# Performance work log

Measured on AMD Instinct MI355X. Metric: run time of the kernel, lower is better.

## Reference

```python
import jax, jax.numpy as jnp
import numpy as np

NUM_EMBEDDINGS = 1024
EMBED_DIM = 256
EMA_DECAY = 0.99
EPS = 1e-05


def setup_inputs() -> dict:
    key = jax.random.key(0)
    k1, k2, k3 = jax.random.split(key, 3)
    B, D, H, W = 32, EMBED_DIM, 32, 32
    z = jax.random.normal(k1, (B, D, H, W), dtype=jnp.float32)
    # torch init: uniform(-1/K, 1/K)
    scale = 1.0 / NUM_EMBEDDINGS
    embedding = jax.random.uniform(k2, (NUM_EMBEDDINGS, EMBED_DIM), dtype=jnp.float32,
                                   minval=-scale, maxval=scale)
    ema_cluster_size = jnp.zeros((NUM_EMBEDDINGS,), dtype=jnp.float32)
    # buffer initialized to a copy of the embedding weights
    ema_embed_sum = embedding.copy()
    return {"z": z, "embedding": embedding,
            "ema_cluster_size": ema_cluster_size, "ema_embed_sum": ema_embed_sum}


def reference(z, embedding, ema_cluster_size, ema_embed_sum):
    B, D, H, W = z.shape
    K = embedding.shape[0]
    # (B, D, H, W) -> (N, D) with N = B*H*W
    z_flat = jnp.transpose(z, (0, 2, 3, 1)).reshape(-1, D)
    # squared L2 distances: ||z||^2 - 2 z E^T + ||e||^2  -> (N, K)
    distances = (jnp.sum(z_flat * z_flat, axis=1, keepdims=True)
                 - 2.0 * z_flat @ embedding.T
                 + jnp.sum(embedding * embedding, axis=1)[None, :])
    indices = jnp.argmin(distances, axis=1)  # (N,) int32
    z_q = embedding[indices].reshape(B, H, W, D).transpose(0, 3, 1, 2)  # (B, D, H, W)

    # training-mode EMA updates (pure functional: return new buffers / codebook)
    ones = jnp.ones((z_flat.shape[0],), dtype=z_flat.dtype)
    counts = jax.ops.segment_sum(ones, indices, num_segments=K)          # (K,)
    embed_sum = jax.ops.segment_sum(z_flat, indices, num_segments=K)     # (K, D)
    new_cs = EMA_DECAY * ema_cluster_size + (1.0 - EMA_DECAY) * counts
    new_es = EMA_DECAY * ema_embed_sum + (1.0 - EMA_DECAY) * embed_sum
    n = jnp.sum(new_cs)
    cluster_size = (new_cs + EPS) / (n + K * EPS) * n
    new_embedding = new_es / cluster_size[:, None]

    # commitment loss and straight-through estimator
    commitment_loss = jnp.mean((z - jax.lax.stop_gradient(z_q)) ** 2)
    z_q_st = z + jax.lax.stop_gradient(z_q - z)
    indices_grid = indices.reshape(B, H, W)
    return (z_q_st, commitment_loss, indices_grid, new_embedding, new_cs, new_es)
```

## Files before the change

kernel.cpp:

```cpp
#include <hip/hip_runtime.h>

#define D_  256
#define K_  1024
#define HW_ 1024
#define N_  32768

#define WS_COUNTS  262144
#define WS_EMBSUM  266240
#define WS_LOSS    1314816
#define WS_NSUM    1314820
#define WS_ENMAX   1314824
#define WS_ZERO0   262144
#define WS_ZEROLEN 1052684
#define WS_NEWCS   1314828
#define WS_ENORM   1318924
#define WS_E16     1454096
#define WS_TOTAL   1978384

#define O_ZQ   0
#define O_LOSS 8388608
#define O_IDX  8388609
#define O_EMB  8421377
#define O_NCS  8683521
#define O_NES  8684545

typedef unsigned short u16;
typedef _Float16 f16x8 __attribute__((ext_vector_type(8)));
typedef float f32x4 __attribute__((ext_vector_type(4)));

__device__ __forceinline__ unsigned f16x2pack(float a, float b) {
  union { _Float16 h; unsigned short u; } ca, cb;
  ca.h = (_Float16)a; cb.h = (_Float16)b;
  return (unsigned)ca.u | ((unsigned)cb.u << 16);
}

__device__ __forceinline__ float pw256_sq(const float* __restrict__ p, int stride) {
  float tot0 = 0.f, tot1 = 0.f;
#pragma unroll
  for (int h = 0; h < 2; ++h) {
    const float* q = p + h * 128 * stride;
    float r[8];
#pragma unroll
    for (int j = 0; j < 8; ++j) { float x = q[j * stride]; r[j] = __fmul_rn(x, x); }
    for (int i = 8; i < 128; i += 8)
#pragma unroll
      for (int j = 0; j < 8; ++j) {
        float x = q[(i + j) * stride];
        r[j] = __fadd_rn(r[j], __fmul_rn(x, x));
      }
    float s = __fadd_rn(__fadd_rn(__fadd_rn(r[0], r[1]), __fadd_rn(r[2], r[3])),
                        __fadd_rn(__fadd_rn(r[4], r[5]), __fadd_rn(r[6], r[7])));
    if (h == 0) tot0 = s; else tot1 = s;
  }
  return __fadd_rn(tot0, tot1);
}

__global__ void vq_eprep(const float* __restrict__ E, float* __restrict__ enorm,
                         u16* __restrict__ E16, unsigned* __restrict__ enmax) {
  int k = blockIdx.x * 256 + threadIdx.x;
  float v = pw256_sq(E + k * D_, 1);
  enorm[k] = v;
  atomicMax(enmax, __float_as_uint(v));
  unsigned* E16w = (unsigned*)E16;
  for (int wd = k; wd < (K_ * D_ / 2); wd += 1024) {
    float2 x = *(const float2*)(E + 2 * wd);
    E16w[wd] = f16x2pack(512.0f * x.x, 512.0f * x.y);
  }
}

template <int CTRL>
__device__ __forceinline__ float dppmin(float v) {
  int p = __builtin_amdgcn_update_dpp(0, __float_as_int(v), CTRL, 0xF, 0xF, true);
  return fminf(v, __int_as_float(p));
}

__device__ __forceinline__ void exact_update(
    const float* zrow, const float* __restrict__ E, int t, int c,
    const float* zn_s, const float* en_s, unsigned long long* best_s) {
  const float* ep = E + c * D_;
  float a = 0.f;
  for (int d0 = 0; d0 < 256; d0 += 8) {
    f32x4 z0 = *(const f32x4*)(zrow + d0);
    f32x4 z1 = *(const f32x4*)(zrow + d0 + 4);
    float4 e0 = *(const float4*)(ep + d0);
    float4 e1 = *(const float4*)(ep + d0 + 4);
    a = __fmaf_rn(z0[0], e0.x, a); a = __fmaf_rn(z0[1], e0.y, a);
    a = __fmaf_rn(z0[2], e0.z, a); a = __fmaf_rn(z0[3], e0.w, a);
    a = __fmaf_rn(z1[0], e1.x, a); a = __fmaf_rn(z1[1], e1.y, a);
    a = __fmaf_rn(z1[2], e1.z, a); a = __fmaf_rn(z1[3], e1.w, a);
  }
  float s = __fadd_rn(__fsub_rn(zn_s[t], __fmul_rn(2.0f, a)), en_s[c]);
  unsigned long long key = ((unsigned long long)__float_as_uint(s) << 32) | (unsigned)c;
  atomicMin(&best_s[t], key);
}

#define TCAP 96
#define ZP  260

__global__ __launch_bounds__(256, 4) void vq_main(
    const float* __restrict__ z, const float* __restrict__ E,
    const u16* __restrict__ E16, const float* __restrict__ enorm,
    const unsigned* __restrict__ enmax,
    float* __restrict__ embsum, float* __restrict__ loss_sum,
    float* __restrict__ counts, float* __restrict__ out_zq,
    float* __restrict__ out_idx) {
  __shared__ __align__(16) float zs[32 * ZP];
  __shared__ float en_s[K_];
  __shared__ float zn_s[32];
  __shared__ float mg_s[32];
  __shared__ unsigned rmin_s[32];
  __shared__ unsigned long long best_s[32];
  __shared__ unsigned tcount[4];
  __shared__ unsigned tlist[4][TCAP];
  __shared__ float wred[4];

  const int tid = threadIdx.x;
  const int tile = blockIdx.x;
  const int bimg = tile >> 5;
  const int hw0 = (tile & 31) << 5;
  const float* zb = z + bimg * (D_ * HW_) + hw0;
  const int n0 = bimg * HW_ + hw0;

#pragma unroll
  for (int r = 0; r < 8; ++r) {
    int ii = r * 256 + tid;
    int d = ii >> 3, t4 = (ii & 7) * 4;
    float4 v = *(const float4*)(zb + d * HW_ + t4);
    zs[(t4 + 0) * ZP + d] = v.x; zs[(t4 + 1) * ZP + d] = v.y;
    zs[(t4 + 2) * ZP + d] = v.z; zs[(t4 + 3) * ZP + d] = v.w;
  }
  for (int i = tid; i < K_; i += 256) en_s[i] = enorm[i];
  if (tid < 4) tcount[tid] = 0;
  __syncthreads();
  if (tid < 32) {
    float zn = pw256_sq(&zs[tid * ZP], 1);
    zn_s[tid] = zn;
    float em = __uint_as_float(*enmax);
    mg_s[tid] = 0.00390625f * sqrtf(zn * em) + 5e-4f;
    rmin_s[tid] = 0xFFFFFFFFu;
    best_s[tid] = ~0ull;
  }
  __syncthreads();

  const int lane = tid & 63;
  const int w = tid >> 6;
  const int l15 = lane & 15, g = lane >> 4;
  const int cw = w * 256;
  const u16* Eb = E16 + (unsigned)(cw + l15) * D_ + g * 8;

  f16x8 efA[2], efB[2];
#pragma unroll
  for (int n = 0; n < 2; ++n)
    efA[n] = *(const f16x8*)(Eb + n * 16 * D_);

  f32x4 acc[2][2];

#define MSTEP(S, EFU, EFF, SN)                                                   \
  {                                                                              \
    const int kk_ = (S) & 7;                                                     \
    {                                                                            \
      const int cn_ = (SN) >> 3, kn_ = (SN) & 7;                                 \
      _Pragma("unroll")                                                          \
      for (int n = 0; n < 2; ++n)                                                \
        EFF[n] = *(const f16x8*)(Eb + (cn_ * 32 + n * 16) * D_ + kn_ * 32);      \
    }                                                                            \
    f16x8 zf_[2];                                                                \
    _Pragma("unroll")                                                            \
    for (int m = 0; m < 2; ++m) {                                                \
      const float* zr = zs + (m * 16 + l15) * ZP + kk_ * 32 + g * 8;             \
      f32x4 lo = *(const f32x4*)zr;                                              \
      f32x4 hi = *(const f32x4*)(zr + 4);                                        \
      f16x8 zc;                                                                  \
      _Pragma("unroll")                                                          \
      for (int j = 0; j < 4; ++j) {                                              \
        zc[j] = (_Float16)lo[j]; zc[4 + j] = (_Float16)hi[j];                    \
      }                                                                          \
      zf_[m] = zc;                                                               \
    }                                                                            \
    _Pragma("unroll")                                                            \
    for (int m = 0; m < 2; ++m)                                                  \
      _Pragma("unroll")                                                          \
      for (int n = 0; n < 2; ++n)                                                \
        acc[m][n] = __builtin_amdgcn_mfma_f32_16x16x32_f16(zf_[m], EFU[n],       \
                                                           acc[m][n], 0, 0, 0);  \
  }

  for (int s2 = 0; s2 < 64; s2 += 2) {
    if ((s2 & 7) == 0) {
      f32x4 z4 = {0.f, 0.f, 0.f, 0.f};
#pragma unroll
      for (int m = 0; m < 2; ++m)
#pragma unroll
        for (int n = 0; n < 2; ++n) acc[m][n] = z4;
    }
    MSTEP(s2, efA, efB, s2 + 1)
    MSTEP(s2 + 1, efB, efA, (s2 + 2) & 63)
    if ((s2 & 7) == 6) {
      const int cb = cw + (s2 >> 3) * 32;
      float enc[2];
#pragma unroll
      for (int n = 0; n < 2; ++n) enc[n] = en_s[cb + n * 16 + l15];
#pragma unroll
      for (int m = 0; m < 2; ++m)
#pragma unroll
        for (int n = 0; n < 2; ++n)
#pragma unroll
          for (int r = 0; r < 4; ++r)
            acc[m][n][r] = __builtin_fmaf(-0.00390625f, acc[m][n][r], enc[n]);
#pragma unroll
      for (int m = 0; m < 2; ++m)
#pragma unroll
        for (int r = 0; r < 4; ++r) {
          float v = fminf(acc[m][0][r], acc[m][1][r]);
          v = dppmin<0xB1>(v);
          v = dppmin<0x4E>(v);
          v = dppmin<0x141>(v);
          v = dppmin<0x140>(v);
          if (l15 == 0) atomicMin(&rmin_s[m * 16 + g * 4 + r], __float_as_uint(v + 4.0f));
        }
#pragma unroll
      for (int m = 0; m < 2; ++m)
#pragma unroll
        for (int r = 0; r < 4; ++r) {
          int t = m * 16 + g * 4 + r;
          float thr = (__uint_as_float(rmin_s[t]) - 4.0f) + mg_s[t];
#pragma unroll
          for (int n = 0; n < 2; ++n) {
            if (acc[m][n][r] <= thr) {
              unsigned pos = atomicAdd(&tcount[w], 1u);
              if (pos < TCAP)
                tlist[w][pos] = ((unsigned)t << 16) | (unsigned)(cb + n * 16 + l15);
            }
          }
        }
    }
  }
#undef MSTEP

  {
    unsigned cnt = tcount[w];
    if (cnt <= TCAP) {
      for (unsigned basei = 0; basei < cnt; basei += 64) {
        unsigned i = basei + (unsigned)lane;
        if (i < cnt) {
          unsigned e = tlist[w][i];
          int t = (int)(e >> 16), c = (int)(e & 1023u);
          exact_update(&zs[t * ZP], E, t, c, zn_s, en_s, best_s);
        }
      }
    } else {
      for (unsigned i = (unsigned)lane; i < 32u * 256u; i += 64) {
        int t = (int)(i >> 8), c = cw + (int)(i & 255u);
        exact_update(&zs[t * ZP], E, t, c, zn_s, en_s, best_s);
      }
    }
  }
  __syncthreads();

  if (tid < 32) {
    int k = (int)(best_s[tid] & 1023ull);
    out_idx[n0 + tid] = (float)k;
    atomicAdd(&counts[k], 1.0f);
  }
  float lsum = 0.f;
  for (int tt = 0; tt < 8; ++tt) {
    int t = w * 8 + tt;
    int k = (int)(best_s[t] & 1023ull);
    const float* Er = E + k * D_;
    float* es = embsum + k * D_;
#pragma unroll
    for (int i = 0; i < 4; ++i) {
      int d = i * 64 + lane;
      float e = Er[d];
      float zv = zs[t * ZP + d];
      float df = __fsub_rn(zv, e);
      lsum += df * df;
      zs[t * ZP + d] = __fadd_rn(zv, __fsub_rn(e, zv));
      atomicAdd(es + d, zv);
    }
  }
#pragma unroll
  for (int o = 32; o > 0; o >>= 1) lsum += __shfl_down(lsum, o, 64);
  if (lane == 0) wred[w] = lsum;
  __syncthreads();
  if (tid == 0) atomicAdd(loss_sum, wred[0] + wred[1] + wred[2] + wred[3]);

  float* ob = out_zq + bimg * (D_ * HW_) + hw0;
#pragma unroll 4
  for (int r = 0; r < 32; ++r) {
    int d = r * 8 + (tid >> 5);
    int t = tid & 31;
    ob[d * HW_ + t] = zs[t * ZP + d];
  }
}

__global__ void vq_newcs_v7(const float* __restrict__ cs_in, const float* __restrict__ counts,
                            float* __restrict__ newcs, float* __restrict__ nsum,
                            const float* __restrict__ loss_sum,
                            float* __restrict__ out_loss, float* __restrict__ out_ncs) {
  int k = blockIdx.x * 256 + threadIdx.x;
  float v = __fadd_rn(__fmul_rn(0.99f, cs_in[k]), __fmul_rn(0.01f, counts[k]));
  newcs[k] = v;
  out_ncs[k] = v;
  float s = v;
#pragma unroll
  for (int o = 32; o > 0; o >>= 1) s += __shfl_down(s, o, 64);
  __shared__ float w[4];
  if ((threadIdx.x & 63) == 0) w[threadIdx.x >> 6] = s;
  __syncthreads();
  if (threadIdx.x == 0) atomicAdd(nsum, w[0] + w[1] + w[2] + w[3]);
  if (k == 0) out_loss[0] = loss_sum[0] * (1.0f / 8388608.0f);
}

__global__ void vq_newemb_v7(const float* __restrict__ es_in, const float* __restrict__ embsum,
                             const float* __restrict__ newcs, const float* __restrict__ nsum,
                             float* __restrict__ out_emb, float* __restrict__ out_nes) {
  int k = blockIdx.x, d = threadIdx.x;
  float n = *nsum;
  float cs = (newcs[k] + 1e-5f) / (n + 1024.0f * 1e-5f) * n;
  float es = __fadd_rn(__fmul_rn(0.99f, es_in[k * D_ + d]),
                       __fmul_rn(0.01f, embsum[k * D_ + d]));
  out_nes[k * D_ + d] = es;
  out_emb[k * D_ + d] = es / cs;
}

extern "C" void kernel_launch(void* const* d_in, const int* in_sizes, int n_in,
                              void* d_out, int out_size, void* d_ws, size_t ws_size,
                              hipStream_t stream) {
  (void)in_sizes; (void)n_in; (void)out_size; (void)ws_size;
  const float* z       = (const float*)d_in[0];
  const float* E       = (const float*)d_in[1];
  const float* ema_cs  = (const float*)d_in[2];
  const float* ema_es  = (const float*)d_in[3];
  float* out = (float*)d_out;
  char* ws = (char*)d_ws;
  float* counts = (float*)(ws + WS_COUNTS);
  float* embsum = (float*)(ws + WS_EMBSUM);
  float* loss_s = (float*)(ws + WS_LOSS);
  float* nsum   = (float*)(ws + WS_NSUM);
  unsigned* enmax = (unsigned*)(ws + WS_ENMAX);
  float* newcs  = (float*)(ws + WS_NEWCS);
  float* enorm  = (float*)(ws + WS_ENORM);
  u16*   e16    = (u16*)(ws + WS_E16);

  hipMemsetAsync(ws + WS_ZERO0, 0, WS_ZEROLEN, stream);
  vq_eprep<<<dim3(4), dim3(256), 0, stream>>>(E, enorm, e16, enmax);
  vq_main<<<dim3(1024), dim3(256), 0, stream>>>(z, E, e16, enorm, enmax,
                                                embsum, loss_s, counts,
                                                out + O_ZQ, out + O_IDX);
  vq_newcs_v7<<<dim3(4), dim3(256), 0, stream>>>(ema_cs, counts, newcs, nsum, loss_s,
                                                 out + O_LOSS, out + O_NCS);
  vq_newemb_v7<<<dim3(K_), dim3(256), 0, stream>>>(ema_es, embsum, newcs, nsum,
                                                   out + O_EMB, out + O_NES);
}
```

Before: 233.1 us.

## Enlarge token tile to 64 with 8 waves and pre-packed fp16 z in LDS

The main kernel now processes 64 tokens per block with 512 threads, and each wave covers 128 codes instead of 256. The z tile is converted to fp16 once and stored in an MFMA-ready LDS layout, which removes the per-step float-to-half conversion. The exact-distance and epilogue paths now read z straight from global memory instead of keeping a float tile in LDS. The embedding prep kernel runs on more blocks. This increases reuse of each E16 fragment across tokens and reduces LDS use, at the cost of more global z reads in the refine and epilogue phases and different occupancy.

Measured after the change: 629.6 us. 170% more time.

```diff
diff --git a/kernel.cpp b/kernel.cpp
--- a/kernel.cpp
+++ b/kernel.cpp
@@ -57,12 +57,14 @@
 
 __global__ void vq_eprep(const float* __restrict__ E, float* __restrict__ enorm,
                          u16* __restrict__ E16, unsigned* __restrict__ enmax) {
-  int k = blockIdx.x * 256 + threadIdx.x;
-  float v = pw256_sq(E + k * D_, 1);
-  enorm[k] = v;
-  atomicMax(enmax, __float_as_uint(v));
+  int gid = blockIdx.x * 256 + threadIdx.x;
+  if (gid < K_) {
+    float v = pw256_sq(E + gid * D_, 1);
+    enorm[gid] = v;
+    atomicMax(enmax, __float_as_uint(v));
+  }
   unsigned* E16w = (unsigned*)E16;
-  for (int wd = k; wd < (K_ * D_ / 2); wd += 1024) {
+  for (int wd = gid; wd < (K_ * D_ / 2); wd += 8192) {
     float2 x = *(const float2*)(E + 2 * wd);
     E16w[wd] = f16x2pack(512.0f * x.x, 512.0f * x.y);
   }
@@ -75,19 +77,21 @@
 }
 
 __device__ __forceinline__ void exact_update(
-    const float* zrow, const float* __restrict__ E, int t, int c,
+    const float* __restrict__ zb, const float* __restrict__ E, int t, int c,
     const float* zn_s, const float* en_s, unsigned long long* best_s) {
+  const float* zp = zb + t;
   const float* ep = E + c * D_;
   float a = 0.f;
   for (int d0 = 0; d0 < 256; d0 += 8) {
-    f32x4 z0 = *(const f32x4*)(zrow + d0);
-    f32x4 z1 = *(const f32x4*)(zrow + d0 + 4);
+    float zr[8];
+#pragma unroll
+    for (int j = 0; j < 8; ++j) zr[j] = zp[(d0 + j) * HW_];
     float4 e0 = *(const float4*)(ep + d0);
     float4 e1 = *(const float4*)(ep + d0 + 4);
-    a = __fmaf_rn(z0[0], e0.x, a); a = __fmaf_rn(z0[1], e0.y, a);
-    a = __fmaf_rn(z0[2], e0.z, a); a = __fmaf_rn(z0[3], e0.w, a);
-    a = __fmaf_rn(z1[0], e1.x, a); a = __fmaf_rn(z1[1], e1.y, a);
-    a = __fmaf_rn(z1[2], e1.z, a); a = __fmaf_rn(z1[3], e1.w, a);
+    a = __fmaf_rn(zr[0], e0.x, a); a = __fmaf_rn(zr[1], e0.y, a);
+    a = __fmaf_rn(zr[2], e0.z, a); a = __fmaf_rn(zr[3], e0.w, a);
+    a = __fmaf_rn(zr[4], e1.x, a); a = __fmaf_rn(zr[5], e1.y, a);
+    a = __fmaf_rn(zr[6], e1.z, a); a = __fmaf_rn(zr[7], e1.w, a);
   }
   float s = __fadd_rn(__fsub_rn(zn_s[t], __fmul_rn(2.0f, a)), en_s[c]);
   unsigned long long key = ((unsigned long long)__float_as_uint(s) << 32) | (unsigned)c;
@@ -95,57 +99,64 @@
 }
 
 #define TCAP 96
-#define ZP  260
-
-__global__ __launch_bounds__(256, 4) void vq_main(
+
+__global__ __launch_bounds__(512, 4) void vq_main(
     const float* __restrict__ z, const float* __restrict__ E,
     const u16* __restrict__ E16, const float* __restrict__ enorm,
     const unsigned* __restrict__ enmax,
     float* __restrict__ embsum, float* __restrict__ loss_sum,
     float* __restrict__ counts, float* __restrict__ out_zq,
     float* __restrict__ out_idx) {
-  __shared__ __align__(16) float zs[32 * ZP];
+  __shared__ __align__(16) u16 zt[32 * 64 * 8];
   __shared__ float en_s[K_];
-  __shared__ float zn_s[32];
-  __shared__ float mg_s[32];
-  __shared__ unsigned rmin_s[32];
-  __shared__ unsigned long long best_s[32];
-  __shared__ unsigned tcount[4];
-  __shared__ unsigned tlist[4][TCAP];
-  __shared__ float wred[4];
+  __shared__ float zn_s[64];
+  __shared__ float mg_s[64];
+  __shared__ unsigned rmin_s[64];
+  __shared__ unsigned long long best_s[64];
+  __shared__ unsigned tcount[8];
+  __shared__ unsigned tlist[8][TCAP];
+  __shared__ float wred[8];
 
   const int tid = threadIdx.x;
   const int tile = blockIdx.x;
-  const int bimg = tile >> 5;
-  const int hw0 = (tile & 31) << 5;
+  const int bimg = tile >> 4;
+  const int hw0 = (tile & 15) << 6;
   const float* zb = z + bimg * (D_ * HW_) + hw0;
   const int n0 = bimg * HW_ + hw0;
 
-#pragma unroll
-  for (int r = 0; r < 8; ++r) {
-    int ii = r * 256 + tid;
-    int d = ii >> 3, t4 = (ii & 7) * 4;
-    float4 v = *(const float4*)(zb + d * HW_ + t4);
-    zs[(t4 + 0) * ZP + d] = v.x; zs[(t4 + 1) * ZP + d] = v.y;
-    zs[(t4 + 2) * ZP + d] = v.z; zs[(t4 + 3) * ZP + d] = v.w;
-  }
-  for (int i = tid; i < K_; i += 256) en_s[i] = enorm[i];
-  if (tid < 4) tcount[tid] = 0;
-  __syncthreads();
-  if (tid < 32) {
-    float zn = pw256_sq(&zs[tid * ZP], 1);
+  if (tid < 64) {
+    float zn = pw256_sq(zb + tid, HW_);
     zn_s[tid] = zn;
     float em = __uint_as_float(*enmax);
     mg_s[tid] = 0.00390625f * sqrtf(zn * em) + 5e-4f;
     rmin_s[tid] = 0xFFFFFFFFu;
     best_s[tid] = ~0ull;
   }
+  if (tid < 8) tcount[tid] = 0;
+  for (int i = tid; i < K_; i += 512) en_s[i] = enorm[i];
+
+  {
+    const int tok = tid & 63;
+    const int kbase = (tid >> 6) * 4;
+    for (int r = 0; r < 4; ++r) {
+      int kb = kbase + r;
+      unsigned pk[4];
+#pragma unroll
+      for (int j = 0; j < 4; ++j) {
+        float x0 = zb[(kb * 8 + 2 * j) * HW_ + tok];
+        float x1 = zb[(kb * 8 + 2 * j + 1) * HW_ + tok];
+        pk[j] = f16x2pack(x0, x1);
+      }
+      uint4 wv; wv.x = pk[0]; wv.y = pk[1]; wv.z = pk[2]; wv.w = pk[3];
+      *(uint4*)(zt + kb * 512 + tok * 8) = wv;
+    }
+  }
   __syncthreads();
 
   const int lane = tid & 63;
   const int w = tid >> 6;
   const int l15 = lane & 15, g = lane >> 4;
-  const int cw = w * 256;
+  const int cw = w * 128;
   const u16* Eb = E16 + (unsigned)(cw + l15) * D_ + g * 8;
 
   f16x8 efA[2], efB[2];
@@ -153,7 +164,7 @@
   for (int n = 0; n < 2; ++n)
     efA[n] = *(const f16x8*)(Eb + n * 16 * D_);
 
-  f32x4 acc[2][2];
+  f32x4 acc[4][2];
 
 #define MSTEP(S, EFU, EFF, SN)                                                   \
   {                                                                              \
@@ -164,51 +175,42 @@
       for (int n = 0; n < 2; ++n)                                                \
         EFF[n] = *(const f16x8*)(Eb + (cn_ * 32 + n * 16) * D_ + kn_ * 32);      \
     }                                                                            \
-    f16x8 zf_[2];                                                                \
+    f16x8 zf_[4];                                                                \
     _Pragma("unroll")                                                            \
-    for (int m = 0; m < 2; ++m) {                                                \
-      const float* zr = zs + (m * 16 + l15) * ZP + kk_ * 32 + g * 8;             \
-      f32x4 lo = *(const f32x4*)zr;                                              \
-      f32x4 hi = *(const f32x4*)(zr + 4);                                        \
-      f16x8 zc;                                                                  \
-      _Pragma("unroll")                                                          \
-      for (int j = 0; j < 4; ++j) {                                              \
-        zc[j] = (_Float16)lo[j]; zc[4 + j] = (_Float16)hi[j];                    \
-      }                                                                          \
-      zf_[m] = zc;                                                               \
-    }                                                                            \
+    for (int m = 0; m < 4; ++m)                                                  \
+      zf_[m] = *(const f16x8*)(zt + (kk_ * 4 + g) * 512 + (m * 16 + l15) * 8);   \
     _Pragma("unroll")                                                            \
-    for (int m = 0; m < 2; ++m)                                                  \
+    for (int m = 0; m < 4; ++m)                                                  \
       _Pragma("unroll")                                                          \
       for (int n = 0; n < 2; ++n)                                                \
         acc[m][n] = __builtin_amdgcn_mfma_f32_16x16x32_f16(zf_[m], EFU[n],       \
                                                            acc[m][n], 0, 0, 0);  \
   }
 
-  for (int s2 = 0; s2 < 64; s2 += 2) {
+  for (int s2 = 0; s2 < 32; s2 += 2) {
     if ((s2 & 7) == 0) {
       f32x4 z4 = {0.f, 0.f, 0.f, 0.f};
 #pragma unroll
-      for (int m = 0; m < 2; ++m)
+      for (int m = 0; m < 4; ++m)
 #pragma unroll
         for (int n = 0; n < 2; ++n) acc[m][n] = z4;
     }
     MSTEP(s2, efA, efB, s2 + 1)
-    MSTEP(s2 + 1, efB, efA, (s2 + 2) & 63)
+    MSTEP(s2 + 1, efB, efA, (s2 + 2) & 31)
     if ((s2 & 7) == 6) {
       const int cb = cw + (s2 >> 3) * 32;
       float enc[2];
 #pragma unroll
       for (int n = 0; n < 2; ++n) enc[n] = en_s[cb + n * 16 + l15];
 #pragma unroll
-      for (int m = 0; m < 2; ++m)
+      for (int m = 0; m < 4; ++m)
 #pragma unroll
         for (int n = 0; n < 2; ++n)
 #pragma unroll
           for (int r = 0; r < 4; ++r)
             acc[m][n][r] = __builtin_fmaf(-0.00390625f, acc[m][n][r], enc[n]);
 #pragma unroll
-      for (int m = 0; m < 2; ++m)
+      for (int m = 0; m < 4; ++m)
 #pragma unroll
         for (int r = 0; r < 4; ++r) {
           float v = fminf(acc[m][0][r], acc[m][1][r]);
@@ -219,7 +221,7 @@
           if (l15 == 0) atomicMin(&rmin_s[m * 16 + g * 4 + r], __float_as_uint(v + 4.0f));
         }
 #pragma unroll
-      for (int m = 0; m < 2; ++m)
+      for (int m = 0; m < 4; ++m)
 #pragma unroll
         for (int r = 0; r < 4; ++r) {
           int t = m * 16 + g * 4 + r;
@@ -244,53 +246,46 @@
         unsigned i = basei + (unsigned)lane;
         if (i < cnt) {
           unsigned e = tlist[w][i];
-          int t = (int)(e >> 16), c = (int)(e & 1023u);
-          exact_update(&zs[t * ZP], E, t, c, zn_s, en_s, best_s);
+          exact_update(zb, E, (int)(e >> 16), (int)(e & 1023u), zn_s, en_s, best_s);
         }
       }
     } else {
-      for (unsigned i = (unsigned)lane; i < 32u * 256u; i += 64) {
-        int t = (int)(i >> 8), c = cw + (int)(i & 255u);
-        exact_update(&zs[t * ZP], E, t, c, zn_s, en_s, best_s);
+      for (unsigned i = (unsigned)lane; i < 64u * 128u; i += 64) {
+        exact_update(zb, E, (int)(i >> 7), cw + (int)(i & 127u), zn_s, en_s, best_s);
       }
     }
   }
   __syncthreads();
 
-  if (tid < 32) {
+  if (tid < 64) {
     int k = (int)(best_s[tid] & 1023ull);
     out_idx[n0 + tid] = (float)k;
     atomicAdd(&counts[k], 1.0f);
   }
-  float lsum = 0.f;
-  for (int tt = 0; tt < 8; ++tt) {
-    int t = w * 8 + tt;
-    int k = (int)(best_s[t] & 1023ull);
-    const float* Er = E + k * D_;
-    float* es = embsum + k * D_;
-#pragma unroll
-    for (int i = 0; i < 4; ++i) {
-      int d = i * 64 + lane;
+  {
+    const int myk = (int)(best_s[lane] & 1023ull);
+    const float* Er = E + myk * D_;
+    float* es = embsum + myk * D_;
+    float* ob = out_zq + bimg * (D_ * HW_) + hw0;
+    float lsum = 0.f;
+    for (int dd = 0; dd < 32; ++dd) {
+      int d = w * 32 + dd;
+      float zv = zb[d * HW_ + lane];
       float e = Er[d];
-      float zv = zs[t * ZP + d];
       float df = __fsub_rn(zv, e);
       lsum += df * df;
-      zs[t * ZP + d] = __fadd_rn(zv, __fsub_rn(e, zv));
+      ob[d * HW_ + lane] = __fadd_rn(zv, __fsub_rn(e, zv));
       atomicAdd(es + d, zv);
     }
-  }
-#pragma unroll
-  for (int o = 32; o > 0; o >>= 1) lsum += __shfl_down(lsum, o, 64);
-  if (lane == 0) wred[w] = lsum;
+#pragma unroll
+    for (int o = 32; o > 0; o >>= 1) lsum += __shfl_down(lsum, o, 64);
+    if (lane == 0) wred[w] = lsum;
+  }
   __syncthreads();
-  if (tid == 0) atomicAdd(loss_sum, wred[0] + wred[1] + wred[2] + wred[3]);
-
-  float* ob = out_zq + bimg * (D_ * HW_) + hw0;
-#pragma unroll 4
-  for (int r = 0; r < 32; ++r) {
-    int d = r * 8 + (tid >> 5);
-    int t = tid & 31;
-    ob[d * HW_ + t] = zs[t * ZP + d];
+  if (tid == 0) {
+    float s = ((wred[0] + wred[1]) + (wred[2] + wred[3])) +
+              ((wred[4] + wred[5]) + (wred[6] + wred[7]));
+    atomicAdd(loss_sum, s);
   }
 }
 
@@ -344,10 +339,10 @@
   u16*   e16    = (u16*)(ws + WS_E16);
 
   hipMemsetAsync(ws + WS_ZERO0, 0, WS_ZEROLEN, stream);
-  vq_eprep<<<dim3(4), dim3(256), 0, stream>>>(E, enorm, e16, enmax);
-  vq_main<<<dim3(1024), dim3(256), 0, stream>>>(z, E, e16, enorm, enmax,
-                                                embsum, loss_s, counts,
-                                                out + O_ZQ, out + O_IDX);
+  vq_eprep<<<dim3(32), dim3(256), 0, stream>>>(E, enorm, e16, enmax);
+  vq_main<<<dim3(512), dim3(512), 0, stream>>>(z, E, e16, enorm, enmax,
+                                               embsum, loss_s, counts,
+                                               out + O_ZQ, out + O_IDX);
   vq_newcs_v7<<<dim3(4), dim3(256), 0, stream>>>(ema_cs, counts, newcs, nsum, loss_s,
                                                  out + O_LOSS, out + O_NCS);
   vq_newemb_v7<<<dim3(K_), dim3(256), 0, stream>>>(ema_es, embsum, newcs, nsum,
```
